# Kernel tuning notes

Hardware: AMD Instinct MI355X
Metric: run time of the kernel (lower is better)

Reference implementation:

```python
import jax, jax.numpy as jnp
import numpy as np
from jax import lax

N = 100000   # nodes
E = 3200000  # edges
D = 10       # feature dim (input_dim == output_dim == 10)
H = 16       # hidden dim of gnn1


def setup_inputs() -> dict:
    key = jax.random.key(0)
    ks = jax.random.split(key, 12)
    def g(k, shape, scale=0.1):
        return jax.random.normal(k, shape, jnp.float32) * scale
    return {
        "x": jax.random.normal(ks[0], (N, D), jnp.float32),
        "edge_index": jax.random.randint(ks[1], (2, E), 0, N, dtype=jnp.int32),
        "W1": g(ks[2], (D, H)),   # gnn1 weight
        "b1": jnp.zeros((H,), jnp.float32),
        "W2": g(ks[3], (H, D)),   # gnn2 weight
        "b2": jnp.zeros((D,), jnp.float32),
        "cW1": g(ks[4], (16, 1, 3)),   # Conv1d(1,16,3) OIH
        "cb1": jnp.zeros((16,), jnp.float32),
        "cW2": g(ks[5], (32, 16, 3)),  # Conv1d(16,32,3) OIH
        "cb2": jnp.zeros((32,), jnp.float32),
        "Wout": g(ks[6], (64, 2)),     # Linear(64, 2)
        "bout": jnp.zeros((2,), jnp.float32),
    }


def gcn_conv(x, src, dst, W, b, n):
    h = x @ W                                       # [N, F_out]
    loop = jnp.arange(n, dtype=src.dtype)
    s = jnp.concatenate([src, loop])
    d = jnp.concatenate([dst, loop])
    deg = jax.ops.segment_sum(jnp.ones(s.shape, h.dtype), d, num_segments=n)
    dinv = lax.rsqrt(jnp.maximum(deg, 1e-12))
    norm = dinv[s] * dinv[d]                        # [E+N]
    msg = h[s] * norm[:, None]                      # gather + scale
    out = jax.ops.segment_sum(msg, d, num_segments=n)  # scatter-add
    return out + b


def conv_block(x, W, b):
    # Conv1d(k=3, stride=1, pad=1) + ReLU + MaxPool1d(2)
    y = lax.conv_general_dilated(x, W, (1,), [(1, 1)],
                                 dimension_numbers=("NCH", "OIH", "NCH"))
    y = jax.nn.relu(y + b[None, :, None])
    return lax.reduce_window(y, -jnp.inf, lax.max, (1, 1, 2), (1, 1, 2), "VALID")


def reference(x, edge_index, W1, b1, W2, b2, cW1, cb1, cW2, cb2, Wout, bout):
    src, dst = edge_index[0], edge_index[1]
    n = x.shape[0]
    x_g = jax.nn.relu(gcn_conv(x, src, dst, W1, b1, n))
    # F.dropout with training=False is identity (eval mode)
    x_g = gcn_conv(x_g, src, dst, W2, b2, n)
    x_dual = x + x_g                                # residual add
    y = x_dual[:, None, :]                          # [N, 1, 10]
    y = conv_block(y, cW1, cb1)                     # [N, 16, 5]
    y = conv_block(y, cW2, cb2)                     # [N, 32, 2]
    y = y.reshape(n, -1)                            # [N, 64]
    out = y @ Wout + bout                           # [N, 2]
    return jax.nn.softmax(out, axis=1)
```

## Files before the change

### kernel.cpp

```cpp
#include <hip/hip_runtime.h>
#include <hip/hip_fp16.h>
#include <math.h>

#define TPB 256
#define TPB_C 512
#define NB_E 512
#define NITER_C 13
#define NPB 256
#define NBKT_CAP 512
#define BKT_STRIDE 8960
#define CHUNK_CAP 6272
#define GA_NODES 32

__global__ __launch_bounds__(TPB_C) void placeP_kernel(const int* __restrict__ ei, int E, int chunk, int nbkt,
                              int* __restrict__ gcur, unsigned* __restrict__ pairs) {
    __shared__ unsigned stg[CHUNK_CAP];
    __shared__ int lh[NBKT_CAP];
    __shared__ int lsc[NBKT_CAP];
    __shared__ int lcur[NBKT_CAP];
    __shared__ int gbase[NBKT_CAP];
    int blk = blockIdx.x;
    int t = threadIdx.x;
    lh[t] = 0;
    __syncthreads();
    int beg = blk * chunk;
    int end = beg + chunk; if (end > E) end = E;
    unsigned rs[NITER_C], rd[NITER_C];
#pragma unroll
    for (int i = 0; i < NITER_C; ++i) {
        int k = beg + t + i * TPB_C;
        bool ok = k < end;
        int s = ok ? ei[k] : 0;
        int d = ok ? ei[E + k] : 0;
        rs[i] = (unsigned)s;
        rd[i] = (unsigned)d;
        if (ok) atomicAdd(&lh[d >> 8], 1);
    }
    __syncthreads();
    int h = lh[t];
    lsc[t] = h;
    __syncthreads();
    for (int off = 1; off < NBKT_CAP; off <<= 1) {
        int v = (t >= off) ? lsc[t - off] : 0;
        __syncthreads();
        lsc[t] += v;
        __syncthreads();
    }
    lcur[t] = lsc[t] - h;
    if (t < nbkt && h > 0) gbase[t] = atomicAdd(&gcur[t], h);
    __syncthreads();
#pragma unroll
    for (int i = 0; i < NITER_C; ++i) {
        int k = beg + t + i * TPB_C;
        if (k < end) {
            int pos = atomicAdd(&lcur[rd[i] >> 8], 1);
            stg[pos] = (rs[i] << 8) | (rd[i] & 255u);
        }
    }
    __syncthreads();
    int grp = t >> 4, lane = t & 15;
    for (int b = grp; b < nbkt; b += TPB_C / 16) {
        int len = lh[b];
        if (len == 0) continue;
        int ls = lsc[b] - len;
        int gb = gbase[b];
        int cap = BKT_STRIDE - gb;
        if (len > cap) len = (cap > 0) ? cap : 0;
        unsigned* dst = pairs + (size_t)b * BKT_STRIDE + gb;
        for (int i = lane; i < len; i += 16)
            dst[i] = stg[ls + i];
    }
}

__global__ __launch_bounds__(TPB) void sortD_kernel(unsigned* __restrict__ pairs,
                                                    const int* __restrict__ gcur, int N,
                                                    int2* __restrict__ rowbd,
                                                    float* __restrict__ dinv,
                                                    const float* __restrict__ x,
                                                    const float* __restrict__ W1,
                                                    __half* __restrict__ g1h) {
    __shared__ unsigned sp[BKT_STRIDE];
    __shared__ int lh[NPB];
    __shared__ int lsc[NPB];
    __shared__ int lcur[NPB];
    __shared__ float sW1[160];
    int b = blockIdx.x;
    size_t rbase = (size_t)b * BKT_STRIDE;
    int cnt = gcur[b];
    if (cnt > BKT_STRIDE) cnt = BKT_STRIDE;
    if (threadIdx.x < 160) sW1[threadIdx.x] = W1[threadIdx.x];
    for (int k = threadIdx.x; k < cnt; k += TPB) sp[k] = pairs[rbase + k];
    lh[threadIdx.x] = 0;
    __syncthreads();
    for (int k = threadIdx.x; k < cnt; k += TPB) atomicAdd(&lh[sp[k] & 255], 1);
    __syncthreads();
    int myh = lh[threadIdx.x];
    lsc[threadIdx.x] = myh;
    __syncthreads();
    for (int off = 1; off < NPB; off <<= 1) {
        int v = (threadIdx.x >= off) ? lsc[threadIdx.x - off] : 0;
        __syncthreads();
        lsc[threadIdx.x] += v;
        __syncthreads();
    }
    int excl = lsc[threadIdx.x] - myh;
    lcur[threadIdx.x] = excl;
    int v = b * NPB + threadIdx.x;
    float dv = rsqrtf((float)myh + 1.0f);
    if (v < N) {
        rowbd[v] = make_int2((int)(rbase + excl), myh);
        dinv[v] = dv;
    }
    __syncthreads();
    for (int k = threadIdx.x; k < cnt; k += TPB) {
        unsigned p = sp[k];
        int pos = atomicAdd(&lcur[p & 255], 1);
        pairs[rbase + pos] = p >> 8;
    }
    if (v < N) {
        float xv[10];
#pragma unroll
        for (int i = 0; i < 10; ++i) xv[i] = x[(size_t)v * 10 + i];
        float o[16];
#pragma unroll
        for (int j = 0; j < 16; ++j) {
            float hh = 0.f;
#pragma unroll
            for (int i = 0; i < 10; ++i) hh = fmaf(xv[i], sW1[i * 16 + j], hh);
            o[j] = hh * dv;
        }
        unsigned u[8];
#pragma unroll
        for (int q = 0; q < 8; ++q) {
            __half2 hh = __floats2half2_rn(o[2 * q], o[2 * q + 1]);
            u[q] = *reinterpret_cast<unsigned*>(&hh);
        }
        uint4* gp = (uint4*)(g1h + (size_t)v * 16);
        gp[0] = make_uint4(u[0], u[1], u[2], u[3]);
        gp[1] = make_uint4(u[4], u[5], u[6], u[7]);
    }
}

__device__ __forceinline__ void acc8(uint4 q, float* a) {
    __half2 h0 = *reinterpret_cast<__half2*>(&q.x);
    __half2 h1 = *reinterpret_cast<__half2*>(&q.y);
    __half2 h2 = *reinterpret_cast<__half2*>(&q.z);
    __half2 h3 = *reinterpret_cast<__half2*>(&q.w);
    float2 f0 = __half22float2(h0), f1 = __half22float2(h1);
    float2 f2 = __half22float2(h2), f3 = __half22float2(h3);
    a[0] += f0.x; a[1] += f0.y; a[2] += f1.x; a[3] += f1.y;
    a[4] += f2.x; a[5] += f2.y; a[6] += f3.x; a[7] += f3.y;
}

__device__ __forceinline__ void gather_core(int beg, int end, const unsigned* srcs,
                                            const uint4* gq, int pair, int half, float* a) {
#pragma unroll
    for (int i = 0; i < 8; ++i) a[i] = 0.f;
    int k = beg + pair;
    for (; k + 4 < end; k += 8) {
        unsigned s0 = srcs[k];
        unsigned s1 = srcs[k + 4];
        uint4 q0 = gq[(size_t)s0 * 2 + half];
        uint4 q1 = gq[(size_t)s1 * 2 + half];
        acc8(q0, a);
        acc8(q1, a);
    }
    if (k < end) acc8(gq[(size_t)srcs[k] * 2 + half], a);
#pragma unroll
    for (int i = 0; i < 8; ++i) a[i] += __shfl_xor(a[i], 2);
#pragma unroll
    for (int i = 0; i < 8; ++i) a[i] += __shfl_xor(a[i], 4);
}

__global__ __launch_bounds__(TPB) void gatherA_kernel(const int2* __restrict__ rowbd, const unsigned* __restrict__ srcs,
                               const uint4* __restrict__ g1q, const float* __restrict__ dinv,
                               const float* __restrict__ b1, const float* __restrict__ W2,
                               __half* __restrict__ g2h, int N) {
    __shared__ float sxg[GA_NODES][17];
    __shared__ float sdinv[GA_NODES];
    __shared__ float sW2[160];
    __shared__ float sb1[16];
    if (threadIdx.x < 160) sW2[threadIdx.x] = W2[threadIdx.x];
    if (threadIdx.x < 16) sb1[threadIdx.x] = b1[threadIdx.x];
    int grp = threadIdx.x >> 3;
    int lane8 = threadIdx.x & 7;
    int pair = lane8 >> 1, half = lane8 & 1;
    int v = blockIdx.x * GA_NODES + grp;
    float a[8];
    if (v < N) {
        int2 bd = rowbd[v];
        gather_core(bd.x, bd.x + bd.y, srcs, g1q, pair, half, a);
        if (lane8 < 2) {
            acc8(g1q[(size_t)v * 2 + half], a);
            float dv = dinv[v];
#pragma unroll
            for (int i = 0; i < 8; ++i)
                sxg[grp][half * 8 + i] = fmaxf(fmaf(dv, a[i], sb1[half * 8 + i]), 0.f);
            if (half == 0) sdinv[grp] = dv;
        }
    }
    __syncthreads();
    for (int idx = threadIdx.x; idx < GA_NODES * 16; idx += TPB) {
        int l2 = idx >> 4, i = idx & 15;
        int v2 = blockIdx.x * GA_NODES + l2;
        if (v2 < N) {
            float val = 0.f;
            if (i < 10) {
                float acc = 0.f;
#pragma unroll
                for (int jj = 0; jj < 16; ++jj) acc = fmaf(sxg[l2][jj], sW2[jj * 10 + i], acc);
                val = acc * sdinv[l2];
            }
            g2h[(size_t)v2 * 16 + i] = __float2half(val);
        }
    }
}

__global__ __launch_bounds__(TPB) void gatherBF_kernel(const int2* __restrict__ rowbd, const unsigned* __restrict__ srcs,
                               const uint4* __restrict__ g2q, const float* __restrict__ x,
                               const float* __restrict__ dinv, const float* __restrict__ b2,
                               const float* __restrict__ cW1, const float* __restrict__ cb1,
                               const float* __restrict__ cW2, const float* __restrict__ cb2,
                               const float* __restrict__ Wout, const float* __restrict__ bout,
                               float* __restrict__ out, int N) {
    __shared__ float sacc[GA_NODES][17];
    __shared__ float sdinv[GA_NODES];
    __shared__ float sp1[GA_NODES][113];
    __shared__ float s_cW1[48];
    __shared__ float s_cb1[16];
    __shared__ float s_cW2[1536];
    __shared__ float s_cb2[32];
    __shared__ float s_Wout[128];
    __shared__ float s_b2[10];
    __shared__ float s_bout[2];
    for (int i = threadIdx.x; i < 1536; i += TPB) s_cW2[i] = cW2[i];
    if (threadIdx.x < 48) s_cW1[threadIdx.x] = cW1[threadIdx.x];
    if (threadIdx.x < 16) s_cb1[threadIdx.x] = cb1[threadIdx.x];
    if (threadIdx.x < 32) s_cb2[threadIdx.x] = cb2[threadIdx.x];
    if (threadIdx.x < 128) s_Wout[threadIdx.x] = Wout[threadIdx.x];
    if (threadIdx.x < 10) s_b2[threadIdx.x] = b2[threadIdx.x];
    if (threadIdx.x < 2) s_bout[threadIdx.x] = bout[threadIdx.x];

    int grp = threadIdx.x >> 3;
    int lane8 = threadIdx.x & 7;
    int pair = lane8 >> 1, half = lane8 & 1;
    int v = blockIdx.x * GA_NODES + grp;
    if (v < N) {
        float a[8];
        int2 bd = rowbd[v];
        gather_core(bd.x, bd.x + bd.y, srcs, g2q, pair, half, a);
        if (lane8 < 2) {
            acc8(g2q[(size_t)v * 2 + half], a);
#pragma unroll
            for (int i = 0; i < 8; ++i) sacc[grp][half * 8 + i] = a[i];
            if (half == 0) sdinv[grp] = dinv[v];
        }
    }
    __syncthreads();
    if (v < N) {
        float dv = sdinv[grp];
        float xd[12];
        xd[0] = 0.f; xd[11] = 0.f;
#pragma unroll
        for (int i = 0; i < 10; ++i)
            xd[i + 1] = x[(size_t)v * 10 + i] + fmaf(dv, sacc[grp][i], s_b2[i]);
#pragma unroll
        for (int q = 0; q < 2; ++q) {
            int c = lane8 * 2 + q;
            float w0 = s_cW1[c * 3 + 0], w1 = s_cW1[c * 3 + 1], w2 = s_cW1[c * 3 + 2];
            float bc = s_cb1[c];
            sp1[grp][c * 7 + 0] = 0.f;
            sp1[grp][c * 7 + 6] = 0.f;
#pragma unroll
            for (int jj = 0; jj < 5; ++jj) {
                float y0 = fmaxf(fmaf(w0, xd[2 * jj + 0], fmaf(w1, xd[2 * jj + 1], fmaf(w2, xd[2 * jj + 2], bc))), 0.f);
                float y1 = fmaxf(fmaf(w0, xd[2 * jj + 1], fmaf(w1, xd[2 * jj + 2], fmaf(w2, xd[2 * jj + 3], bc))), 0.f);
                sp1[grp][c * 7 + jj + 1] = fmaxf(y0, y1);
            }
        }
    }
    __syncthreads();
    if (v < N) {
        float z0 = 0.f, z1 = 0.f;
#pragma unroll
        for (int q = 0; q < 4; ++q) {
            int o = lane8 * 4 + q;
            float y2[5];
#pragma unroll
            for (int i = 0; i < 5; ++i) y2[i] = s_cb2[o];
#pragma unroll
            for (int c = 0; c < 16; ++c) {
                float w0 = s_cW2[o * 48 + c * 3 + 0];
                float w1 = s_cW2[o * 48 + c * 3 + 1];
                float w2 = s_cW2[o * 48 + c * 3 + 2];
#pragma unroll
                for (int i = 0; i < 5; ++i)
                    y2[i] = fmaf(w0, sp1[grp][c * 7 + i], fmaf(w1, sp1[grp][c * 7 + i + 1], fmaf(w2, sp1[grp][c * 7 + i + 2], y2[i])));
            }
            float p20 = fmaxf(fmaxf(y2[0], 0.f), fmaxf(y2[1], 0.f));
            float p21 = fmaxf(fmaxf(y2[2], 0.f), fmaxf(y2[3], 0.f));
            z0 = fmaf(p20, s_Wout[(o * 2 + 0) * 2 + 0], z0);
            z1 = fmaf(p20, s_Wout[(o * 2 + 0) * 2 + 1], z1);
            z0 = fmaf(p21, s_Wout[(o * 2 + 1) * 2 + 0], z0);
            z1 = fmaf(p21, s_Wout[(o * 2 + 1) * 2 + 1], z1);
        }
        z0 += __shfl_xor(z0, 1); z1 += __shfl_xor(z1, 1);
        z0 += __shfl_xor(z0, 2); z1 += __shfl_xor(z1, 2);
        z0 += __shfl_xor(z0, 4); z1 += __shfl_xor(z1, 4);
        if (lane8 == 0) {
            z0 += s_bout[0];
            z1 += s_bout[1];
            float m = fmaxf(z0, z1);
            float e0 = expf(z0 - m), e1 = expf(z1 - m);
            float inv = 1.f / (e0 + e1);
            ((float2*)out)[v] = make_float2(e0 * inv, e1 * inv);
        }
    }
}

extern "C" void kernel_launch(void* const* d_in, const int* in_sizes, int n_in,
                              void* d_out, int out_size, void* d_ws, size_t ws_size,
                              hipStream_t stream) {
    const float* x    = (const float*)d_in[0];
    const int*   ei   = (const int*)d_in[1];
    const float* W1   = (const float*)d_in[2];
    const float* b1   = (const float*)d_in[3];
    const float* W2   = (const float*)d_in[4];
    const float* b2   = (const float*)d_in[5];
    const float* cW1  = (const float*)d_in[6];
    const float* cb1  = (const float*)d_in[7];
    const float* cW2  = (const float*)d_in[8];
    const float* cb2  = (const float*)d_in[9];
    const float* Wout = (const float*)d_in[10];
    const float* bout = (const float*)d_in[11];
    float* out = (float*)d_out;

    int N = in_sizes[0] / 10;
    int E = in_sizes[1] / 2;
    int nbkt = (N + NPB - 1) / NPB;
    int chunk = (E + NB_E - 1) / NB_E;
    (void)nbkt;

    char* p = (char*)d_ws;
    int*      gcur  = (int*)p;       p += sizeof(int) * NBKT_CAP;
    unsigned* pairs = (unsigned*)p;  p += sizeof(unsigned) * (size_t)NBKT_CAP * BKT_STRIDE;
    int2*     rowbd = (int2*)p;      p += sizeof(int2) * (size_t)N;
    float*    dinv  = (float*)p;     p += sizeof(float) * (size_t)N;
    __half*   g1h   = (__half*)p;    p += sizeof(__half) * (size_t)16 * N;
    __half*   g2h   = (__half*)p;    p += sizeof(__half) * (size_t)16 * N;

    hipMemsetAsync(gcur, 0, sizeof(int) * NBKT_CAP, stream);
    placeP_kernel<<<NB_E, TPB_C, 0, stream>>>(ei, E, chunk, nbkt, gcur, pairs);
    sortD_kernel<<<nbkt, TPB, 0, stream>>>(pairs, gcur, N, rowbd, dinv, x, W1, g1h);

    int ga = (N + GA_NODES - 1) / GA_NODES;
    gatherA_kernel<<<ga, TPB, 0, stream>>>(rowbd, pairs, (const uint4*)g1h, dinv, b1, W2, g2h, N);
    gatherBF_kernel<<<ga, TPB, 0, stream>>>(rowbd, pairs, (const uint4*)g2h, x, dinv, b2,
                                            cW1, cb1, cW2, cb2, Wout, bout, out, N);
}
```

Measured before the change: 141.8 us.

## Widen placement and sort blocks, unroll gather by four, pad conv weights

Doubles the thread count of the edge-placement kernel to 1024 and cuts its per-thread iterations from 13 to 7. The sort kernel now runs 512 threads per block, with guards so only the first 256 do the per-node work. The gather loop gets a four-way unrolled body so more independent loads are in flight. Conv2 and output weights are stored in shared memory with padded strides to reduce bank conflicts. The wider blocks use more registers and may lower occupancy, and the idle extra threads add synchronisation cost.

```diff
diff --git a/kernel.cpp b/kernel.cpp
--- a/kernel.cpp
+++ b/kernel.cpp
@@ -3,9 +3,10 @@
 #include <math.h>
 
 #define TPB 256
-#define TPB_C 512
+#define TPB_C 1024
+#define TPB_D 512
 #define NB_E 512
-#define NITER_C 13
+#define NITER_C 7
 #define NPB 256
 #define NBKT_CAP 512
 #define BKT_STRIDE 8960
@@ -21,7 +22,7 @@
     __shared__ int gbase[NBKT_CAP];
     int blk = blockIdx.x;
     int t = threadIdx.x;
-    lh[t] = 0;
+    if (t < NBKT_CAP) lh[t] = 0;
     __syncthreads();
     int beg = blk * chunk;
     int end = beg + chunk; if (end > E) end = E;
@@ -37,17 +38,19 @@
         if (ok) atomicAdd(&lh[d >> 8], 1);
     }
     __syncthreads();
-    int h = lh[t];
-    lsc[t] = h;
+    int h = (t < NBKT_CAP) ? lh[t] : 0;
+    if (t < NBKT_CAP) lsc[t] = h;
     __syncthreads();
     for (int off = 1; off < NBKT_CAP; off <<= 1) {
-        int v = (t >= off) ? lsc[t - off] : 0;
+        int v = (t < NBKT_CAP && t >= off) ? lsc[t - off] : 0;
         __syncthreads();
-        lsc[t] += v;
+        if (t < NBKT_CAP) lsc[t] += v;
         __syncthreads();
     }
-    lcur[t] = lsc[t] - h;
-    if (t < nbkt && h > 0) gbase[t] = atomicAdd(&gcur[t], h);
+    if (t < NBKT_CAP) {
+        lcur[t] = lsc[t] - h;
+        if (t < nbkt && h > 0) gbase[t] = atomicAdd(&gcur[t], h);
+    }
     __syncthreads();
 #pragma unroll
     for (int i = 0; i < NITER_C; ++i) {
@@ -72,7 +75,7 @@
     }
 }
 
-__global__ __launch_bounds__(TPB) void sortD_kernel(unsigned* __restrict__ pairs,
+__global__ __launch_bounds__(TPB_D) void sortD_kernel(unsigned* __restrict__ pairs,
                                                     const int* __restrict__ gcur, int N,
                                                     int2* __restrict__ rowbd,
                                                     float* __restrict__ dinv,
@@ -85,39 +88,42 @@
     __shared__ int lcur[NPB];
     __shared__ float sW1[160];
     int b = blockIdx.x;
+    int t = threadIdx.x;
     size_t rbase = (size_t)b * BKT_STRIDE;
     int cnt = gcur[b];
     if (cnt > BKT_STRIDE) cnt = BKT_STRIDE;
-    if (threadIdx.x < 160) sW1[threadIdx.x] = W1[threadIdx.x];
-    for (int k = threadIdx.x; k < cnt; k += TPB) sp[k] = pairs[rbase + k];
-    lh[threadIdx.x] = 0;
-    __syncthreads();
-    for (int k = threadIdx.x; k < cnt; k += TPB) atomicAdd(&lh[sp[k] & 255], 1);
-    __syncthreads();
-    int myh = lh[threadIdx.x];
-    lsc[threadIdx.x] = myh;
+    if (t < 160) sW1[t] = W1[t];
+    for (int k = t; k < cnt; k += TPB_D) sp[k] = pairs[rbase + k];
+    if (t < NPB) lh[t] = 0;
+    __syncthreads();
+    for (int k = t; k < cnt; k += TPB_D) atomicAdd(&lh[sp[k] & 255], 1);
+    __syncthreads();
+    int myh = (t < NPB) ? lh[t] : 0;
+    if (t < NPB) lsc[t] = myh;
     __syncthreads();
     for (int off = 1; off < NPB; off <<= 1) {
-        int v = (threadIdx.x >= off) ? lsc[threadIdx.x - off] : 0;
+        int v = (t < NPB && t >= off) ? lsc[t - off] : 0;
         __syncthreads();
-        lsc[threadIdx.x] += v;
+        if (t < NPB) lsc[t] += v;
         __syncthreads();
     }
-    int excl = lsc[threadIdx.x] - myh;
-    lcur[threadIdx.x] = excl;
-    int v = b * NPB + threadIdx.x;
+    int v = b * NPB + t;
     float dv = rsqrtf((float)myh + 1.0f);
-    if (v < N) {
-        rowbd[v] = make_int2((int)(rbase + excl), myh);
-        dinv[v] = dv;
-    }
-    __syncthreads();
-    for (int k = threadIdx.x; k < cnt; k += TPB) {
+    if (t < NPB) {
+        int excl = lsc[t] - myh;
+        lcur[t] = excl;
+        if (v < N) {
+            rowbd[v] = make_int2((int)(rbase + excl), myh);
+            dinv[v] = dv;
+        }
+    }
+    __syncthreads();
+    for (int k = t; k < cnt; k += TPB_D) {
         unsigned p = sp[k];
         int pos = atomicAdd(&lcur[p & 255], 1);
         pairs[rbase + pos] = p >> 8;
     }
-    if (v < N) {
+    if (t < NPB && v < N) {
         float xv[10];
 #pragma unroll
         for (int i = 0; i < 10; ++i) xv[i] = x[(size_t)v * 10 + i];
@@ -157,13 +163,23 @@
 #pragma unroll
     for (int i = 0; i < 8; ++i) a[i] = 0.f;
     int k = beg + pair;
+    for (; k + 12 < end; k += 16) {
+        unsigned s0 = srcs[k];
+        unsigned s1 = srcs[k + 4];
+        unsigned s2 = srcs[k + 8];
+        unsigned s3 = srcs[k + 12];
+        uint4 q0 = gq[(size_t)s0 * 2 + half];
+        uint4 q1 = gq[(size_t)s1 * 2 + half];
+        uint4 q2 = gq[(size_t)s2 * 2 + half];
+        uint4 q3 = gq[(size_t)s3 * 2 + half];
+        acc8(q0, a); acc8(q1, a); acc8(q2, a); acc8(q3, a);
+    }
     for (; k + 4 < end; k += 8) {
         unsigned s0 = srcs[k];
         unsigned s1 = srcs[k + 4];
         uint4 q0 = gq[(size_t)s0 * 2 + half];
         uint4 q1 = gq[(size_t)s1 * 2 + half];
-        acc8(q0, a);
-        acc8(q1, a);
+        acc8(q0, a); acc8(q1, a);
     }
     if (k < end) acc8(gq[(size_t)srcs[k] * 2 + half], a);
 #pragma unroll
@@ -228,16 +244,16 @@
     __shared__ float sp1[GA_NODES][113];
     __shared__ float s_cW1[48];
     __shared__ float s_cb1[16];
-    __shared__ float s_cW2[1536];
+    __shared__ float s_cW2p[32 * 49];
     __shared__ float s_cb2[32];
-    __shared__ float s_Wout[128];
+    __shared__ float s_Woutp[32 * 5];
     __shared__ float s_b2[10];
     __shared__ float s_bout[2];
-    for (int i = threadIdx.x; i < 1536; i += TPB) s_cW2[i] = cW2[i];
+    for (int i = threadIdx.x; i < 1536; i += TPB) s_cW2p[(i / 48) * 49 + (i % 48)] = cW2[i];
+    if (threadIdx.x < 128) s_Woutp[(threadIdx.x >> 2) * 5 + (threadIdx.x & 3)] = Wout[threadIdx.x];
     if (threadIdx.x < 48) s_cW1[threadIdx.x] = cW1[threadIdx.x];
     if (threadIdx.x < 16) s_cb1[threadIdx.x] = cb1[threadIdx.x];
     if (threadIdx.x < 32) s_cb2[threadIdx.x] = cb2[threadIdx.x];
-    if (threadIdx.x < 128) s_Wout[threadIdx.x] = Wout[threadIdx.x];
     if (threadIdx.x < 10) s_b2[threadIdx.x] = b2[threadIdx.x];
     if (threadIdx.x < 2) s_bout[threadIdx.x] = bout[threadIdx.x];
 
@@ -290,19 +306,19 @@
             for (int i = 0; i < 5; ++i) y2[i] = s_cb2[o];
 #pragma unroll
             for (int c = 0; c < 16; ++c) {
-                float w0 = s_cW2[o * 48 + c * 3 + 0];
-                float w1 = s_cW2[o * 48 + c * 3 + 1];
-                float w2 = s_cW2[o * 48 + c * 3 + 2];
+                float w0 = s_cW2p[o * 49 + c * 3 + 0];
+                float w1 = s_cW2p[o * 49 + c * 3 + 1];
+                float w2 = s_cW2p[o * 49 + c * 3 + 2];
 #pragma unroll
                 for (int i = 0; i < 5; ++i)
                     y2[i] = fmaf(w0, sp1[grp][c * 7 + i], fmaf(w1, sp1[grp][c * 7 + i + 1], fmaf(w2, sp1[grp][c * 7 + i + 2], y2[i])));
             }
             float p20 = fmaxf(fmaxf(y2[0], 0.f), fmaxf(y2[1], 0.f));
             float p21 = fmaxf(fmaxf(y2[2], 0.f), fmaxf(y2[3], 0.f));
-            z0 = fmaf(p20, s_Wout[(o * 2 + 0) * 2 + 0], z0);
-            z1 = fmaf(p20, s_Wout[(o * 2 + 0) * 2 + 1], z1);
-            z0 = fmaf(p21, s_Wout[(o * 2 + 1) * 2 + 0], z0);
-            z1 = fmaf(p21, s_Wout[(o * 2 + 1) * 2 + 1], z1);
+            z0 = fmaf(p20, s_Woutp[o * 5 + 0], z0);
+            z1 = fmaf(p20, s_Woutp[o * 5 + 1], z1);
+            z0 = fmaf(p21, s_Woutp[o * 5 + 2], z0);
+            z1 = fmaf(p21, s_Woutp[o * 5 + 3], z1);
         }
         z0 += __shfl_xor(z0, 1); z1 += __shfl_xor(z1, 1);
         z0 += __shfl_xor(z0, 2); z1 += __shfl_xor(z1, 2);
@@ -339,7 +355,6 @@
     int E = in_sizes[1] / 2;
     int nbkt = (N + NPB - 1) / NPB;
     int chunk = (E + NB_E - 1) / NB_E;
-    (void)nbkt;
 
     char* p = (char*)d_ws;
     int*      gcur  = (int*)p;       p += sizeof(int) * NBKT_CAP;
@@ -351,7 +366,7 @@
 
     hipMemsetAsync(gcur, 0, sizeof(int) * NBKT_CAP, stream);
     placeP_kernel<<<NB_E, TPB_C, 0, stream>>>(ei, E, chunk, nbkt, gcur, pairs);
-    sortD_kernel<<<nbkt, TPB, 0, stream>>>(pairs, gcur, N, rowbd, dinv, x, W1, g1h);
+    sortD_kernel<<<nbkt, TPB_D, 0, stream>>>(pairs, gcur, N, rowbd, dinv, x, W1, g1h);
 
     int ga = (N + GA_NODES - 1) / GA_NODES;
     gatherA_kernel<<<ga, TPB, 0, stream>>>(rowbd, pairs, (const uint4*)g1h, dinv, b1, W2, g2h, N);
```

New measurement: 126.0 us. 11.2% less time.
